# Performance work log

Hardware: AMD Instinct MI355X
Metric: run time of the kernel (lower is better)

## Reference

```python
import jax, jax.numpy as jnp
import numpy as np

EPS = 1e-5
NUM_GN_GROUPS = 32


def setup_inputs() -> dict:
    key = jax.random.key(0)
    k1, k2, k3 = jax.random.split(key, 3)
    B, C, N, G = 2, 256, 4096, 8
    c = C // G
    return {
        "points": jax.random.normal(k1, (B, C, N), dtype=jnp.float32),
        "conv_w": jax.random.normal(k2, (G, c, c), dtype=jnp.float32) / np.sqrt(c),
        "conv_b": jax.random.normal(k3, (C,), dtype=jnp.float32) * 0.02,
        "gn_w": jnp.ones((C,), dtype=jnp.float32),
        "gn_b": jnp.zeros((C,), dtype=jnp.float32),
    }


def reference(points, conv_w, conv_b, gn_w, gn_b):
    B, C, N = points.shape
    G = conv_w.shape[0]
    c = C // G  # channels per attention group
    identity = points

    # grouped 1x1 conv: per-group [c,c] matmul + bias
    x = points.reshape(B, G, c, N)
    x = jnp.einsum('gij,bgjn->bgin', conv_w, x) + conv_b.reshape(1, G, c, 1)

    # attention[b,g,n,m] = sum_i x[b,g,i,n] * x[b,g,i,m] / sqrt(c)
    scale = 1.0 / np.sqrt(c).astype(np.float32)
    attn = jnp.einsum('bgin,bgim->bgnm', x, x) * scale
    # softmax over dim=2 (the query/row N axis -- non-standard)
    attn = jax.nn.softmax(attn, axis=2)

    # ELU-gated second matmul: [B,G,c,N] @ [B,G,N,N] -> [B,G,c,N]
    x = jnp.einsum('bgcn,bgnm->bgcm', jax.nn.elu(x), attn)

    # channel shuffle: [B,G,c,N] -> [B,c,G,N] -> [B,C,N]
    x = x.transpose(0, 2, 1, 3).reshape(B, C, N)
    x = x + identity

    # GroupNorm(32 groups) over (channels-in-group, N)
    xg = x.reshape(B, NUM_GN_GROUPS, C // NUM_GN_GROUPS, N)
    mean = xg.mean(axis=(2, 3), keepdims=True)
    var = xg.var(axis=(2, 3), keepdims=True)
    xg = (xg - mean) * jax.lax.rsqrt(var + EPS)
    x = xg.reshape(B, C, N)
    return x * gn_w.reshape(1, C, 1) + gn_b.reshape(1, C, 1)
```

## Files before the change

kernel.cpp:

```cpp
#include <hip/hip_runtime.h>

typedef __attribute__((ext_vector_type(8))) short bf16x8;
typedef __attribute__((ext_vector_type(4))) short bf16x4;
typedef __attribute__((ext_vector_type(4))) float f32x4;

#if __has_builtin(__builtin_amdgcn_exp2f)
#define EXP2(x) __builtin_amdgcn_exp2f(x)
#else
#define EXP2(x) exp2f(x)
#endif

__device__ __forceinline__ unsigned short f2bf(float f) {
    union { float f; unsigned int u; } v; v.f = f;
    unsigned int r = v.u + 0x7fffu + ((v.u >> 16) & 1u);
    return (unsigned short)(r >> 16);
}

__device__ __forceinline__ float asf(unsigned int u) {
    union { unsigned int u; float f; } v; v.u = u; return v.f;
}

#define QK_PRESCALE 0.50500983f

__global__ __launch_bounds__(256, 4) void conv_kernel(
    const float* __restrict__ points, const float* __restrict__ conv_w,
    const float* __restrict__ conv_b,
    unsigned short* __restrict__ xqT, unsigned short* __restrict__ xv)
{
    __shared__ float w[1024];
    const int h  = blockIdx.x >> 6;
    const int nc = blockIdx.x & 63;
    const int g  = h & 7;
    const int tid = threadIdx.x;
    const float* wg = conv_w + g * 1024;
    for (int k = tid; k < 1024; k += 256) w[k] = wg[k];
    __syncthreads();
    const int n  = nc * 64 + (tid & 63);
    const int ig = tid >> 6;
    const float* p = points + (size_t)h * 32 * 4096 + n;

    float out[8];
#pragma unroll
    for (int ii = 0; ii < 8; ++ii) out[ii] = conv_b[g * 32 + ig * 8 + ii];

    const float4* w4base = (const float4*)(w + ig * 8 * 32);
#pragma unroll 2
    for (int j4 = 0; j4 < 8; ++j4) {
        float pv0 = p[(size_t)(j4 * 4 + 0) * 4096];
        float pv1 = p[(size_t)(j4 * 4 + 1) * 4096];
        float pv2 = p[(size_t)(j4 * 4 + 2) * 4096];
        float pv3 = p[(size_t)(j4 * 4 + 3) * 4096];
#pragma unroll
        for (int ii = 0; ii < 8; ++ii) {
            float4 ww = w4base[ii * 8 + j4];
            out[ii] += ww.x * pv0 + ww.y * pv1 + ww.z * pv2 + ww.w * pv3;
        }
    }

    unsigned short tq[8];
#pragma unroll
    for (int ii = 0; ii < 8; ++ii) tq[ii] = f2bf(out[ii] * QK_PRESCALE);
    *(bf16x8*)(xqT + ((size_t)h * 4096 + n) * 32 + ig * 8) = *(bf16x8*)tq;
#pragma unroll
    for (int ii = 0; ii < 8; ++ii) {
        float x = out[ii];
        float e = x > 0.f ? x : (__expf(x) - 1.f);
        xv[((size_t)h * 32 + ig * 8 + ii) * 4096 + n] = f2bf(e);
    }
}

#define VSTR 136

#if __has_builtin(__builtin_amdgcn_cvt_pk_bf16_f32)
typedef __attribute__((ext_vector_type(2))) __bf16 bf16x2v;
__device__ __forceinline__ bf16x4 exp_pack(f32x4 sc) {
    float e0 = EXP2(sc[0]), e1 = EXP2(sc[1]);
    float e2 = EXP2(sc[2]), e3 = EXP2(sc[3]);
    union { bf16x2v v[2]; bf16x4 s; } u;
    u.v[0] = __builtin_amdgcn_cvt_pk_bf16_f32(e0, e1);
    u.v[1] = __builtin_amdgcn_cvt_pk_bf16_f32(e2, e3);
    return u.s;
}
#else
__device__ __forceinline__ bf16x4 exp_pack(f32x4 sc) {
    union { float f; unsigned int u; } e0, e1, e2, e3;
    e0.f = EXP2(sc[0]); e1.f = EXP2(sc[1]); e2.f = EXP2(sc[2]); e3.f = EXP2(sc[3]);
    unsigned int t0 = e0.u & 0xffff0000u, t1 = e1.u & 0xffff0000u;
    unsigned int t2 = e2.u & 0xffff0000u, t3 = e3.u & 0xffff0000u;
    union { unsigned int d[2]; bf16x4 v; } pk;
    pk.d[0] = (t0 >> 16) | t1;
    pk.d[1] = (t2 >> 16) | t3;
    return pk.v;
}
#endif

#define CHUNK(C0, KU, KP, VH)                                                  \
    {                                                                          \
        *(bf16x8*)((VH) + vi * VSTR + vn)      = va;                           \
        *(bf16x8*)((VH) + vi * VSTR + vn + 64) = vb;                           \
        __syncthreads();                                                       \
        const int pfb = ((C0) + 128) & 4095;                                   \
        va = *(const bf16x8*)(vbase + (size_t)vi * 4096 + pfb + vn);           \
        vb = *(const bf16x8*)(vbase + (size_t)vi * 4096 + pfb + vn + 64);      \
        _Pragma("unroll")                                                      \
        for (int s8 = 0; s8 < 8; ++s8)                                         \
            KP[s8] = *(const bf16x8*)(kfp + (size_t)(pfb + s8 * 16) * 32);     \
        _Pragma("unroll")                                                      \
        for (int sub = 0; sub < 2; ++sub) {                                    \
            union { bf16x4 v; unsigned int d[2]; } E[4];                       \
            _Pragma("unroll")                                                  \
            for (int s = 0; s < 4; ++s) {                                      \
                f32x4 sc = __builtin_amdgcn_mfma_f32_16x16x32_bf16(            \
                    KU[sub * 4 + s], qfrag, (f32x4){0.f, 0.f, 0.f, 0.f},       \
                    0, 0, 0);                                                  \
                E[s].v = exp_pack(sc);                                         \
            }                                                                  \
            union { unsigned int d[4]; bf16x8 v; } F0, F1;                     \
            _Pragma("unroll")                                                  \
            for (int p = 0; p < 2; ++p) {                                      \
                unsigned int a0 = E[0].d[p], b0 = E[1].d[p];                   \
                asm("v_permlane32_swap_b32 %0, %1" : "+v"(a0), "+v"(b0));      \
                asm("v_permlane16_swap_b32 %0, %1" : "+v"(a0), "+v"(b0));      \
                F0.d[p] = a0; F0.d[2 + p] = b0;                                \
                unsigned int a1 = E[2].d[p], b1 = E[3].d[p];                   \
                asm("v_permlane32_swap_b32 %0, %1" : "+v"(a1), "+v"(b1));      \
                asm("v_permlane16_swap_b32 %0, %1" : "+v"(a1), "+v"(b1));      \
                F1.d[p] = a1; F1.d[2 + p] = b1;                                \
            }                                                                  \
            _Pragma("unroll")                                                  \
            for (int ng = 0; ng < 2; ++ng) {                                   \
                bf16x8 pfrag = ng ? F1.v : F0.v;                               \
                const int col = sub * 64 + ng * 32 + quad * 8;                 \
                bf16x8 v0 = *(const bf16x8*)((VH) + l15 * VSTR + col);         \
                bf16x8 v1 = *(const bf16x8*)((VH) + (16 + l15) * VSTR + col);  \
                acc0 = __builtin_amdgcn_mfma_f32_16x16x32_bf16(v0, pfrag,      \
                                                               acc0, 0, 0, 0); \
                acc1 = __builtin_amdgcn_mfma_f32_16x16x32_bf16(v1, pfrag,      \
                                                               acc1, 0, 0, 0); \
                accL = __builtin_amdgcn_mfma_f32_16x16x32_bf16(ones, pfrag,    \
                                                               accL, 0, 0, 0); \
            }                                                                  \
        }                                                                      \
    }

__global__ __launch_bounds__(256, 4) void attn_kernel(
    const unsigned short* __restrict__ xqT,
    const unsigned short* __restrict__ xv,
    const float* __restrict__ points,
    float* __restrict__ z,
    float* __restrict__ part)
{
    __shared__ unsigned short Vt[2][32 * VSTR];

    const int h  = blockIdx.y;
    const int b = h >> 3, g = h & 7;
    const int tid = threadIdx.x;
    const int wv = tid >> 6, lane = tid & 63;
    const int quad = lane >> 4, l15 = lane & 15;

    const int m = blockIdx.x * 64 + wv * 16 + l15;

    const unsigned short* kbase = xqT + (size_t)h * 4096 * 32;
    const unsigned short* vbase = xv  + (size_t)h * 32 * 4096;

    const bf16x8 qfrag = *(const bf16x8*)(kbase + (size_t)m * 32 + quad * 8);

    f32x4 acc0 = {0.f, 0.f, 0.f, 0.f};
    f32x4 acc1 = {0.f, 0.f, 0.f, 0.f};
    f32x4 accL = {0.f, 0.f, 0.f, 0.f};
    const short one_bf = (short)0x3f80;
    const bf16x8 ones = {one_bf, one_bf, one_bf, one_bf,
                         one_bf, one_bf, one_bf, one_bf};

    const int vi = tid >> 3, vn = (tid & 7) * 8;
    unsigned short* Vt0 = &Vt[0][0];
    unsigned short* Vt1 = &Vt[1][0];

    const unsigned short* kfp = kbase + (size_t)l15 * 32 + quad * 8;

    const unsigned short* vptr = vbase + (size_t)vi * 4096 + vn;
    bf16x8 va = *(const bf16x8*)vptr;
    bf16x8 vb = *(const bf16x8*)(vptr + 64);

    bf16x8 kA[8], kB[8];
#pragma unroll
    for (int s8 = 0; s8 < 8; ++s8)
        kA[s8] = *(const bf16x8*)(kfp + (size_t)(s8 * 16) * 32);

    for (int n0 = 0; n0 < 4096; n0 += 256) {
        CHUNK(n0,       kA, kB, Vt0);
        CHUNK(n0 + 128, kB, kA, Vt1);
    }

    const float inv = 1.f / accL[0];

    const float* pb = points + (size_t)b * 256 * 4096;
    float* zb = z + (size_t)b * 256 * 4096;
    float sA[8], ssA[8];
#pragma unroll
    for (int half = 0; half < 2; ++half) {
        f32x4 a = half ? acc1 : acc0;
#pragma unroll
        for (int r = 0; r < 4; ++r) {
            int i = half * 16 + quad * 4 + r;
            size_t off = (size_t)(i * 8 + g) * 4096 + m;
            float zv = a[r] * inv + pb[off];
            zb[off] = zv;
            float s = zv, ss = zv * zv;
#pragma unroll
            for (int d = 1; d < 16; d <<= 1) {
                s  += __shfl_xor(s, d, 64);
                ss += __shfl_xor(ss, d, 64);
            }
            sA[half * 4 + r] = s; ssA[half * 4 + r] = ss;
        }
    }
    __syncthreads();
    float2* Ls = (float2*)&Vt[0][0];
    if (l15 == 0) {
#pragma unroll
        for (int k = 0; k < 8; ++k) {
            int i = (k >> 2) * 16 + quad * 4 + (k & 3);
            Ls[wv * 32 + i] = make_float2(sA[k], ssA[k]);
        }
    }
    __syncthreads();
    if (tid < 32) {
        float2 p0 = Ls[tid], p1 = Ls[32 + tid], p2 = Ls[64 + tid], p3 = Ls[96 + tid];
        float s  = p0.x + p1.x + p2.x + p3.x;
        float ss = p0.y + p1.y + p2.y + p3.y;
        size_t base = ((size_t)(b * 32 + tid)) * 1024 + (size_t)g * 64 + blockIdx.x;
        part[base]       = s;
        part[base + 512] = ss;
    }
}

__global__ __launch_bounds__(256) void gn_apply(float* __restrict__ z,
                                                const float* __restrict__ part,
                                                const float* __restrict__ gw,
                                                const float* __restrict__ gb)
{
    const int tid = threadIdx.x;
    const int idx = blockIdx.x * 256 + tid;
    const int chg = blockIdx.x >> 2;
    const int grp = chg >> 3;
    const int ch  = chg & 255;

    const float* pp = part + (size_t)grp * 1024;
    float s  = pp[tid]       + pp[tid + 256];
    float ss = pp[512 + tid] + pp[768 + tid];
#pragma unroll
    for (int off = 32; off > 0; off >>= 1) {
        s  += __shfl_down(s, off, 64);
        ss += __shfl_down(ss, off, 64);
    }
    __shared__ float red[8];
    if ((tid & 63) == 0) { red[(tid >> 6) * 2] = s; red[(tid >> 6) * 2 + 1] = ss; }
    __syncthreads();
    s  = red[0] + red[2] + red[4] + red[6];
    ss = red[1] + red[3] + red[5] + red[7];

    const float mean = s * (1.f / 32768.f);
    const float var  = ss * (1.f / 32768.f) - mean * mean;
    const float rstd = rsqrtf(var + 1e-5f);
    const float w  = gw[ch] * rstd;
    const float bb = gb[ch] - mean * w;
    float4* p = (float4*)z;
    float4 v = p[idx];
    v.x = v.x * w + bb; v.y = v.y * w + bb;
    v.z = v.z * w + bb; v.w = v.w * w + bb;
    p[idx] = v;
}

extern "C" void kernel_launch(void* const* d_in, const int* in_sizes, int n_in,
                              void* d_out, int out_size, void* d_ws, size_t ws_size,
                              hipStream_t stream)
{
    const float* points = (const float*)d_in[0];
    const float* conv_w = (const float*)d_in[1];
    const float* conv_b = (const float*)d_in[2];
    const float* gn_w   = (const float*)d_in[3];
    const float* gn_b   = (const float*)d_in[4];
    float* out = (float*)d_out;
    char* ws = (char*)d_ws;
    unsigned short* xqT = (unsigned short*)ws;
    unsigned short* xv  = (unsigned short*)(ws + (size_t)4 * 1024 * 1024);
    float* part = (float*)(ws + (size_t)8 * 1024 * 1024);

    conv_kernel<<<1024, 256, 0, stream>>>(points, conv_w, conv_b, xqT, xv);
    attn_kernel<<<dim3(64, 16), 256, 0, stream>>>(xqT, xv, points, out, part);
    gn_apply<<<2048, 256, 0, stream>>>(out, part, gn_w, gn_b);
}
```

Before: 149.1 us.

## Split attention key dimension across two blocks and combine partials in new kernel

Adds a split-K attention kernel that processes each half of the 4096 keys in a separate block (grid z=2), writing unnormalized partial accumulators and row sums to workspace. A new combine kernel sums the two halves, normalizes, adds the residual and computes GroupNorm partial statistics, followed by a simplified gn_apply2. The aim is to double the block count (1024 to 2048) to fill more CUs, at the cost of an extra kernel launch and roughly 16MB of extra fp32 partial traffic. The old path is kept as a fallback when the workspace is too small.

```diff
diff --git a/kernel.cpp b/kernel.cpp
--- a/kernel.cpp
+++ b/kernel.cpp
@@ -94,17 +94,17 @@
 }
 #endif
 
-#define CHUNK(C0, KU, KP, VH)                                                  \
+#define CHUNK(C0, KU, KP, VH, VB, KF, MSK)                                     \
     {                                                                          \
         *(bf16x8*)((VH) + vi * VSTR + vn)      = va;                           \
         *(bf16x8*)((VH) + vi * VSTR + vn + 64) = vb;                           \
         __syncthreads();                                                       \
-        const int pfb = ((C0) + 128) & 4095;                                   \
-        va = *(const bf16x8*)(vbase + (size_t)vi * 4096 + pfb + vn);           \
-        vb = *(const bf16x8*)(vbase + (size_t)vi * 4096 + pfb + vn + 64);      \
+        const int pfb = ((C0) + 128) & (MSK);                                  \
+        va = *(const bf16x8*)((VB) + (size_t)vi * 4096 + pfb + vn);            \
+        vb = *(const bf16x8*)((VB) + (size_t)vi * 4096 + pfb + vn + 64);       \
         _Pragma("unroll")                                                      \
         for (int s8 = 0; s8 < 8; ++s8)                                         \
-            KP[s8] = *(const bf16x8*)(kfp + (size_t)(pfb + s8 * 16) * 32);     \
+            KP[s8] = *(const bf16x8*)((KF) + (size_t)(pfb + s8 * 16) * 32);    \
         _Pragma("unroll")                                                      \
         for (int sub = 0; sub < 2; ++sub) {                                    \
             union { bf16x4 v; unsigned int d[2]; } E[4];                       \
@@ -143,6 +143,67 @@
         }                                                                      \
     }
 
+#define ATTN_PROLOGUE                                                          \
+    const int h  = blockIdx.y;                                                 \
+    const int tid = threadIdx.x;                                               \
+    const int wv = tid >> 6, lane = tid & 63;                                  \
+    const int quad = lane >> 4, l15 = lane & 15;                               \
+    const int m = blockIdx.x * 64 + wv * 16 + l15;                             \
+    const unsigned short* kbase = xqT + (size_t)h * 4096 * 32;                 \
+    const unsigned short* vbase = xv  + (size_t)h * 32 * 4096;                 \
+    const bf16x8 qfrag = *(const bf16x8*)(kbase + (size_t)m * 32 + quad * 8);  \
+    f32x4 acc0 = {0.f, 0.f, 0.f, 0.f};                                         \
+    f32x4 acc1 = {0.f, 0.f, 0.f, 0.f};                                         \
+    f32x4 accL = {0.f, 0.f, 0.f, 0.f};                                         \
+    const short one_bf = (short)0x3f80;                                        \
+    const bf16x8 ones = {one_bf, one_bf, one_bf, one_bf,                       \
+                         one_bf, one_bf, one_bf, one_bf};                      \
+    const int vi = tid >> 3, vn = (tid & 7) * 8;                               \
+    unsigned short* Vt0 = &Vt[0][0];                                           \
+    unsigned short* Vt1 = &Vt[1][0];                                           \
+    const unsigned short* kfp = kbase + (size_t)l15 * 32 + quad * 8;
+
+__global__ __launch_bounds__(256, 4) void attn_split(
+    const unsigned short* __restrict__ xqT,
+    const unsigned short* __restrict__ xv,
+    float* __restrict__ pacc,
+    float* __restrict__ plsum)
+{
+    __shared__ unsigned short Vt[2][32 * VSTR];
+    ATTN_PROLOGUE
+    const int khalf = blockIdx.z;
+    const int kofs  = khalf * 2048;
+    const unsigned short* kfpK   = kfp   + (size_t)kofs * 32;
+    const unsigned short* vbaseK = vbase + kofs;
+
+    const unsigned short* vptr = vbaseK + (size_t)vi * 4096 + vn;
+    bf16x8 va = *(const bf16x8*)vptr;
+    bf16x8 vb = *(const bf16x8*)(vptr + 64);
+
+    bf16x8 kA[8], kB[8];
+#pragma unroll
+    for (int s8 = 0; s8 < 8; ++s8)
+        kA[s8] = *(const bf16x8*)(kfpK + (size_t)(s8 * 16) * 32);
+
+    for (int n0 = 0; n0 < 2048; n0 += 256) {
+        CHUNK(n0,       kA, kB, Vt0, vbaseK, kfpK, 2047);
+        CHUNK(n0 + 128, kB, kA, Vt1, vbaseK, kfpK, 2047);
+    }
+
+    float* pb = pacc + ((size_t)(h * 2 + khalf) * 32) * 4096 + m;
+#pragma unroll
+    for (int half = 0; half < 2; ++half) {
+        f32x4 a = half ? acc1 : acc0;
+#pragma unroll
+        for (int r = 0; r < 4; ++r) {
+            int i = half * 16 + quad * 4 + r;
+            pb[(size_t)i * 4096] = a[r];
+        }
+    }
+    if (quad == 0)
+        plsum[(size_t)(h * 2 + khalf) * 4096 + m] = accL[0];
+}
+
 __global__ __launch_bounds__(256, 4) void attn_kernel(
     const unsigned short* __restrict__ xqT,
     const unsigned short* __restrict__ xv,
@@ -151,32 +212,8 @@
     float* __restrict__ part)
 {
     __shared__ unsigned short Vt[2][32 * VSTR];
-
-    const int h  = blockIdx.y;
+    ATTN_PROLOGUE
     const int b = h >> 3, g = h & 7;
-    const int tid = threadIdx.x;
-    const int wv = tid >> 6, lane = tid & 63;
-    const int quad = lane >> 4, l15 = lane & 15;
-
-    const int m = blockIdx.x * 64 + wv * 16 + l15;
-
-    const unsigned short* kbase = xqT + (size_t)h * 4096 * 32;
-    const unsigned short* vbase = xv  + (size_t)h * 32 * 4096;
-
-    const bf16x8 qfrag = *(const bf16x8*)(kbase + (size_t)m * 32 + quad * 8);
-
-    f32x4 acc0 = {0.f, 0.f, 0.f, 0.f};
-    f32x4 acc1 = {0.f, 0.f, 0.f, 0.f};
-    f32x4 accL = {0.f, 0.f, 0.f, 0.f};
-    const short one_bf = (short)0x3f80;
-    const bf16x8 ones = {one_bf, one_bf, one_bf, one_bf,
-                         one_bf, one_bf, one_bf, one_bf};
-
-    const int vi = tid >> 3, vn = (tid & 7) * 8;
-    unsigned short* Vt0 = &Vt[0][0];
-    unsigned short* Vt1 = &Vt[1][0];
-
-    const unsigned short* kfp = kbase + (size_t)l15 * 32 + quad * 8;
 
     const unsigned short* vptr = vbase + (size_t)vi * 4096 + vn;
     bf16x8 va = *(const bf16x8*)vptr;
@@ -188,8 +225,8 @@
         kA[s8] = *(const bf16x8*)(kfp + (size_t)(s8 * 16) * 32);
 
     for (int n0 = 0; n0 < 4096; n0 += 256) {
-        CHUNK(n0,       kA, kB, Vt0);
-        CHUNK(n0 + 128, kB, kA, Vt1);
+        CHUNK(n0,       kA, kB, Vt0, vbase, kfp, 4095);
+        CHUNK(n0 + 128, kB, kA, Vt1, vbase, kfp, 4095);
     }
 
     const float inv = 1.f / accL[0];
@@ -235,31 +272,71 @@
     }
 }
 
-__global__ __launch_bounds__(256) void gn_apply(float* __restrict__ z,
-                                                const float* __restrict__ part,
-                                                const float* __restrict__ gw,
-                                                const float* __restrict__ gb)
+__global__ __launch_bounds__(256) void combine_kernel(
+    const float* __restrict__ pacc, const float* __restrict__ plsum,
+    const float* __restrict__ points, float* __restrict__ z,
+    float* __restrict__ part)
 {
     const int tid = threadIdx.x;
-    const int idx = blockIdx.x * 256 + tid;
-    const int chg = blockIdx.x >> 2;
-    const int grp = chg >> 3;
-    const int ch  = chg & 255;
-
-    const float* pp = part + (size_t)grp * 1024;
-    float s  = pp[tid]       + pp[tid + 256];
-    float ss = pp[512 + tid] + pp[768 + tid];
+    const int blk = blockIdx.x;
+    const int row = blk >> 2;
+    const int q   = blk & 3;
+    const int b = row >> 8, ch = row & 255;
+    const int i = ch >> 3, g = ch & 7;
+    const int h = b * 8 + g;
+    const int f4 = q * 256 + tid;
+
+    float4 a0 = ((const float4*)pacc)[((size_t)(h * 2 + 0) * 32 + i) * 1024 + f4];
+    float4 a1 = ((const float4*)pacc)[((size_t)(h * 2 + 1) * 32 + i) * 1024 + f4];
+    float4 l0 = ((const float4*)plsum)[(size_t)(h * 2 + 0) * 1024 + f4];
+    float4 l1 = ((const float4*)plsum)[(size_t)(h * 2 + 1) * 1024 + f4];
+    float4 pt = ((const float4*)points)[(size_t)row * 1024 + f4];
+    float4 v;
+    v.x = (a0.x + a1.x) / (l0.x + l1.x) + pt.x;
+    v.y = (a0.y + a1.y) / (l0.y + l1.y) + pt.y;
+    v.z = (a0.z + a1.z) / (l0.z + l1.z) + pt.z;
+    v.w = (a0.w + a1.w) / (l0.w + l1.w) + pt.w;
+    ((float4*)z)[(size_t)row * 1024 + f4] = v;
+
+    float s  = (v.x + v.y) + (v.z + v.w);
+    float ss = (v.x * v.x + v.y * v.y) + (v.z * v.z + v.w * v.w);
 #pragma unroll
     for (int off = 32; off > 0; off >>= 1) {
         s  += __shfl_down(s, off, 64);
         ss += __shfl_down(ss, off, 64);
     }
     __shared__ float red[8];
-    if ((tid & 63) == 0) { red[(tid >> 6) * 2] = s; red[(tid >> 6) * 2 + 1] = ss; }
+    const int w = tid >> 6;
+    if ((tid & 63) == 0) { red[w * 2] = s; red[w * 2 + 1] = ss; }
     __syncthreads();
-    s  = red[0] + red[2] + red[4] + red[6];
-    ss = red[1] + red[3] + red[5] + red[7];
-
+    if (tid == 0) {
+        s  = red[0] + red[2] + red[4] + red[6];
+        ss = red[1] + red[3] + red[5] + red[7];
+        const int grp = b * 32 + i;
+        part[grp * 64 + g * 4 + q]      = s;
+        part[grp * 64 + 32 + g * 4 + q] = ss;
+    }
+}
+
+__global__ __launch_bounds__(256) void gn_apply2(float* __restrict__ z,
+                                                 const float* __restrict__ part,
+                                                 const float* __restrict__ gw,
+                                                 const float* __restrict__ gb)
+{
+    const int tid = threadIdx.x;
+    const int idx = blockIdx.x * 256 + tid;
+    const int chg = idx >> 10;
+    const int grp = chg >> 3;
+    const int ch  = chg & 255;
+
+    const float* pp = part + grp * 64;
+    const int k = tid & 31;
+    float s = pp[k], ss = pp[32 + k];
+#pragma unroll
+    for (int off = 16; off > 0; off >>= 1) {
+        s  += __shfl_xor(s, off, 64);
+        ss += __shfl_xor(ss, off, 64);
+    }
     const float mean = s * (1.f / 32768.f);
     const float var  = ss * (1.f / 32768.f) - mean * mean;
     const float rstd = rsqrtf(var + 1e-5f);
@@ -272,6 +349,43 @@
     p[idx] = v;
 }
 
+__global__ __launch_bounds__(256) void gn_apply(float* __restrict__ z,
+                                                const float* __restrict__ part,
+                                                const float* __restrict__ gw,
+                                                const float* __restrict__ gb)
+{
+    const int tid = threadIdx.x;
+    const int idx = blockIdx.x * 256 + tid;
+    const int chg = idx >> 10;
+    const int grp = chg >> 3;
+    const int ch  = chg & 255;
+
+    const float* pp = part + (size_t)grp * 1024;
+    float s  = pp[tid]       + pp[tid + 256];
+    float ss = pp[512 + tid] + pp[768 + tid];
+#pragma unroll
+    for (int off = 32; off > 0; off >>= 1) {
+        s  += __shfl_down(s, off, 64);
+        ss += __shfl_down(ss, off, 64);
+    }
+    __shared__ float red[8];
+    if ((tid & 63) == 0) { red[(tid >> 6) * 2] = s; red[(tid >> 6) * 2 + 1] = ss; }
+    __syncthreads();
+    s  = red[0] + red[2] + red[4] + red[6];
+    ss = red[1] + red[3] + red[5] + red[7];
+
+    const float mean = s * (1.f / 32768.f);
+    const float var  = ss * (1.f / 32768.f) - mean * mean;
+    const float rstd = rsqrtf(var + 1e-5f);
+    const float w  = gw[ch] * rstd;
+    const float bb = gb[ch] - mean * w;
+    float4* p = (float4*)z;
+    float4 v = p[idx];
+    v.x = v.x * w + bb; v.y = v.y * w + bb;
+    v.z = v.z * w + bb; v.w = v.w * w + bb;
+    p[idx] = v;
+}
+
 extern "C" void kernel_launch(void* const* d_in, const int* in_sizes, int n_in,
                               void* d_out, int out_size, void* d_ws, size_t ws_size,
                               hipStream_t stream)
@@ -285,9 +399,20 @@
     char* ws = (char*)d_ws;
     unsigned short* xqT = (unsigned short*)ws;
     unsigned short* xv  = (unsigned short*)(ws + (size_t)4 * 1024 * 1024);
-    float* part = (float*)(ws + (size_t)8 * 1024 * 1024);
 
     conv_kernel<<<1024, 256, 0, stream>>>(points, conv_w, conv_b, xqT, xv);
-    attn_kernel<<<dim3(64, 16), 256, 0, stream>>>(xqT, xv, points, out, part);
-    gn_apply<<<2048, 256, 0, stream>>>(out, part, gn_w, gn_b);
-}
+
+    const size_t MB = 1024 * 1024;
+    if (ws_size >= 25 * MB) {
+        float* pacc  = (float*)(ws + 8 * MB);
+        float* plsum = (float*)(ws + 24 * MB);
+        float* part  = (float*)(ws + 24 * MB + 512 * 1024);
+        attn_split<<<dim3(64, 16, 2), 256, 0, stream>>>(xqT, xv, pacc, plsum);
+        combine_kernel<<<2048, 256, 0, stream>>>(pacc, plsum, points, out, part);
+        gn_apply2<<<2048, 256, 0, stream>>>(out, part, gn_w, gn_b);
+    } else {
+        float* part = (float*)(ws + 8 * MB);
+        attn_kernel<<<dim3(64, 16), 256, 0, stream>>>(xqT, xv, points, out, part);
+        gn_apply<<<2048, 256, 0, stream>>>(out, part, gn_w, gn_b);
+    }
+}
```

After: 155.1 us. 1.04x slower.
